# Kernel optimization log

Hardware: AMD Instinct MI355X
Metric: run time of the kernel (lower is better)

Reference implementation:

```python
import jax, jax.numpy as jnp
import numpy as np

D_MODEL = 512
N_HEADS = 8
HEAD_DIM = D_MODEL // N_HEADS
SEQ = 2048
BATCH = 2
EPS = 1e-5
SCALE = 1.0 / np.sqrt(HEAD_DIM).astype(np.float32)
# (kind, window, dilation) per head, matching init_kwargs head_specs
SPECS = [("global", 0, 1), ("global", 0, 1),
         ("window", 64, 1), ("window", 128, 1), ("window", 256, 1),
         ("dilated", 64, 2), ("dilated", 64, 4), ("dilated", 64, 8)]


def build_masks(N):
    i = jnp.arange(N)
    D = jnp.abs(i[:, None] - i[None, :])
    ms = []
    for kind, w, dil in SPECS:
        if kind == "global":
            ms.append(jnp.ones((N, N), dtype=bool))
        elif kind == "window":
            ms.append(D <= w)
        else:  # dilated
            ms.append((D % dil == 0) & (D // dil <= w))
    return jnp.stack(ms)  # [H, N, N] bool


def layernorm(x, g, b):
    mu = jnp.mean(x, axis=-1, keepdims=True)
    var = jnp.mean((x - mu) ** 2, axis=-1, keepdims=True)
    return (x - mu) * jax.lax.rsqrt(var + EPS) * g + b


def setup_inputs() -> dict:
    key = jax.random.key(0)
    ks = jax.random.split(key, 7)
    w = 0.02
    return {
        "x": jax.random.normal(ks[0], (BATCH, SEQ, D_MODEL), dtype=jnp.float32),
        "Wq": jax.random.normal(ks[1], (D_MODEL, D_MODEL), dtype=jnp.float32) * w,
        "Wk": jax.random.normal(ks[2], (D_MODEL, D_MODEL), dtype=jnp.float32) * w,
        "Wv": jax.random.normal(ks[3], (D_MODEL, D_MODEL), dtype=jnp.float32) * w,
        "Wo": jax.random.normal(ks[4], (D_MODEL, D_MODEL), dtype=jnp.float32) * w,
        "T_w1": jax.random.normal(ks[5], (D_MODEL, D_MODEL), dtype=jnp.float32) * w,
        "T_b1": jnp.zeros((D_MODEL,), dtype=jnp.float32),
        "T_w2": jax.random.normal(ks[6], (1, D_MODEL), dtype=jnp.float32) * w,
        "T_b2": jnp.zeros((1,), dtype=jnp.float32),
        "ln_in_g": jnp.ones((D_MODEL,), dtype=jnp.float32),
        "ln_in_b": jnp.zeros((D_MODEL,), dtype=jnp.float32),
        "ln_out_g": jnp.ones((D_MODEL,), dtype=jnp.float32),
        "ln_out_b": jnp.zeros((D_MODEL,), dtype=jnp.float32),
    }


def reference(x, Wq, Wk, Wv, Wo, T_w1, T_b1, T_w2, T_b2,
              ln_in_g, ln_in_b, ln_out_g, ln_out_b):
    B, N, H = x.shape
    x0 = x
    xn = layernorm(x, ln_in_g, ln_in_b)
    # torch Linear: y = x @ W.T ; reshape to [B, h, N, d]
    def heads(W):
        return (xn @ W.T).reshape(B, N, N_HEADS, HEAD_DIM).transpose(0, 2, 1, 3)
    Q, K, V = heads(Wq), heads(Wk), heads(Wv)
    attn = jnp.einsum("bhqd,bhkd->bhqk", Q, K) * SCALE
    mask = build_masks(N)  # [h, N, N]
    attn = jnp.where(mask[None], attn, -jnp.inf)
    attn = jax.nn.softmax(attn, axis=-1)  # every row has diagonal unmasked
    out = jnp.einsum("bhqk,bhkd->bhqd", attn, V)
    out = out.transpose(0, 2, 1, 3).reshape(B, N, N_HEADS * HEAD_DIM)
    out = out @ Wo.T
    # tanh-gated softmax over sequence dim
    T_logits = jnp.tanh(xn @ T_w1.T + T_b1) @ T_w2.T + T_b2  # [B, N, 1]
    T = jax.nn.softmax(T_logits, axis=1)
    out = out * T
    return layernorm(out + x0, ln_out_g, ln_out_b)
```

## Files before the change

kernel.cpp:

```cpp
#include <hip/hip_runtime.h>
#include <math.h>

#define N_SEQ 2048
#define DM    512
#define NTOK  4096
#define NH    8
#define HD    64
#define NSLOT 18

typedef __attribute__((ext_vector_type(8))) short short8;
typedef __attribute__((ext_vector_type(4))) short short4_t;
typedef __attribute__((ext_vector_type(4))) float f32x4;

__device__ inline short f2bf(float x) {
    union { float f; unsigned u; } v; v.f = x;
    unsigned r = v.u + 0x7fff + ((v.u >> 16) & 1);
    return (short)(r >> 16);
}
__device__ inline float bf2f(short s) {
    union { unsigned u; float f; } v; v.u = ((unsigned)(unsigned short)s) << 16;
    return v.f;
}
__device__ inline unsigned pkbf(float a, float b) {
    return ((unsigned)(unsigned short)f2bf(b) << 16) | (unsigned)(unsigned short)f2bf(a);
}
__device__ inline float ftanh(float x) {
    float e = __expf(2.f * x);
    return 1.f - 2.f / (e + 1.f);
}

__device__ inline f32x4 mfma16(short8 a, short8 b, f32x4 c) {
    return __builtin_amdgcn_mfma_f32_16x16x32_bf16(a, b, c, 0, 0, 0);
}

__device__ __forceinline__ void async_cp16(const short* g, short* l) {
    __builtin_amdgcn_global_load_lds(
        (const __attribute__((address_space(1))) void*)g,
        (__attribute__((address_space(3))) void*)l, 16, 0, 0);
}

__global__ __launch_bounds__(256) void k_lncvt(
    const float* __restrict__ x, const float* __restrict__ g,
    const float* __restrict__ b, short* __restrict__ y, float* __restrict__ lg,
    const float* __restrict__ Wq, const float* __restrict__ Wk,
    const float* __restrict__ Wv, const float* __restrict__ Tw1,
    const float* __restrict__ Wo,
    short* __restrict__ wcat, short* __restrict__ wo) {
    int blk = blockIdx.x, t = threadIdx.x;
    if (blk < 2048) {
        int sub = t >> 7, tt = t & 127;
        int tk = blk * 2 + sub;
        if (tt == 0) lg[tk] = 0.f;
        float4 xv = ((const float4*)(x + (size_t)tk * DM))[tt];
        float s = xv.x + xv.y + xv.z + xv.w;
        float q = xv.x*xv.x + xv.y*xv.y + xv.z*xv.z + xv.w*xv.w;
        for (int o = 32; o; o >>= 1) { s += __shfl_down(s, o); q += __shfl_down(q, o); }
        __shared__ float ls[4], lq[4];
        if ((t & 63) == 0) { ls[t >> 6] = s; lq[t >> 6] = q; }
        __syncthreads();
        s = ls[sub * 2] + ls[sub * 2 + 1];
        q = lq[sub * 2] + lq[sub * 2 + 1];
        float mu = s * (1.f / DM);
        float var = q * (1.f / DM) - mu * mu;
        float rs = rsqrtf(var + 1e-5f);
        float4 gv = ((const float4*)g)[tt], bv = ((const float4*)b)[tt];
        short4_t o;
        o[0] = f2bf((xv.x - mu) * rs * gv.x + bv.x);
        o[1] = f2bf((xv.y - mu) * rs * gv.y + bv.y);
        o[2] = f2bf((xv.z - mu) * rs * gv.z + bv.z);
        o[3] = f2bf((xv.w - mu) * rs * gv.w + bv.w);
        *(short4_t*)&y[(size_t)tk * DM + tt * 4] = o;
    } else {
        int id = (blk - 2048) * 256 + t;
        if (id < 262144) {
            int z = id >> 16; int off = id & 65535;
            const float* s = (z == 0) ? Wq : (z == 1) ? Wk : (z == 2) ? Wv : Tw1;
            float4 v = ((const float4*)s)[off];
            short4_t o = {f2bf(v.x), f2bf(v.y), f2bf(v.z), f2bf(v.w)};
            *(short4_t*)(wcat + (size_t)z * 262144 + (size_t)off * 4) = o;
        } else {
            int off = id - 262144;
            float4 v = ((const float4*)Wo)[off];
            short4_t o = {f2bf(v.x), f2bf(v.y), f2bf(v.z), f2bf(v.w)};
            *(short4_t*)(wo + (size_t)off * 4) = o;
        }
    }
}

__global__ __launch_bounds__(256) void k_gemmqkvt(
    const short* __restrict__ A, const short* __restrict__ W,
    const float* __restrict__ Tb1, const float* __restrict__ Tw2,
    short* __restrict__ qb, short* __restrict__ kb, short* __restrict__ vtb,
    float* __restrict__ lg) {
    __shared__ short As[128 * 32];
    __shared__ short Bs[128 * 32];
    int t = threadIdx.x;
    int lane = t & 63, w = t >> 6;
    int wy = w >> 1, wx = w & 1;
    int ln = lane & 15, q4 = lane >> 4;
    int c0 = blockIdx.x * 128, m0 = blockIdx.y * 128;
    int sr = t >> 2, sc = (t & 3) << 3;
    f32x4 acc[4][4];
    f32x4 zero = {0.f, 0.f, 0.f, 0.f};
    #pragma unroll
    for (int i = 0; i < 4; i++)
        #pragma unroll
        for (int j = 0; j < 4; j++) acc[i][j] = zero;
    for (int k0 = 0; k0 < DM; k0 += 32) {
        __syncthreads();
        async_cp16(&A[(size_t)(m0 + sr) * DM + k0 + sc],      &As[sr * 32 + sc]);
        async_cp16(&A[(size_t)(m0 + 64 + sr) * DM + k0 + sc], &As[(64 + sr) * 32 + sc]);
        async_cp16(&W[(size_t)(c0 + sr) * DM + k0 + sc],      &Bs[sr * 32 + sc]);
        async_cp16(&W[(size_t)(c0 + 64 + sr) * DM + k0 + sc], &Bs[(64 + sr) * 32 + sc]);
        __syncthreads();
        short8 af[4], bfr[4];
        #pragma unroll
        for (int i = 0; i < 4; i++)
            af[i] = *(short8*)&As[(wy * 64 + i * 16 + ln) * 32 + q4 * 8];
        #pragma unroll
        for (int j = 0; j < 4; j++)
            bfr[j] = *(short8*)&Bs[(wx * 64 + j * 16 + ln) * 32 + q4 * 8];
        #pragma unroll
        for (int i = 0; i < 4; i++)
            #pragma unroll
            for (int j = 0; j < 4; j++)
                acc[i][j] = mfma16(af[i], bfr[j], acc[i][j]);
    }
    int z = c0 >> 9;
    if (z < 2) {
        short* dst = (z == 0) ? qb : kb;
        float sc2 = (z == 0) ? 0.125f : 1.0f;
        #pragma unroll
        for (int i = 0; i < 4; i++)
            #pragma unroll
            for (int j = 0; j < 4; j++)
                #pragma unroll
                for (int r = 0; r < 4; r++) {
                    int row = m0 + wy * 64 + i * 16 + q4 * 4 + r;
                    int col = c0 + wx * 64 + j * 16 + ln;
                    int nin = col & 511;
                    int h = nin >> 6, d = nin & 63;
                    int bi = row >> 11, n = row & (N_SEQ - 1);
                    dst[(((size_t)bi * NH + h) * N_SEQ + n) * HD + d] =
                        f2bf(acc[i][j][r] * sc2);
                }
    } else if (z == 2) {
        #pragma unroll
        for (int i = 0; i < 4; i++) {
            int row0 = m0 + wy * 64 + i * 16 + q4 * 4;
            int bi = row0 >> 11, n0 = row0 & (N_SEQ - 1);
            #pragma unroll
            for (int j = 0; j < 4; j++) {
                int nin = (c0 + wx * 64 + j * 16 + ln) & 511;
                int h = nin >> 6, d = nin & 63;
                short4_t o = {f2bf(acc[i][j][0]), f2bf(acc[i][j][1]),
                              f2bf(acc[i][j][2]), f2bf(acc[i][j][3])};
                *(short4_t*)&vtb[(((size_t)bi * NH + h) * HD + d) * N_SEQ + n0] = o;
            }
        }
    } else {
        #pragma unroll
        for (int i = 0; i < 4; i++) {
            #pragma unroll
            for (int r = 0; r < 4; r++) {
                float s = 0.f;
                #pragma unroll
                for (int j = 0; j < 4; j++) {
                    int tc = (c0 & 511) + wx * 64 + j * 16 + ln;
                    s += ftanh(acc[i][j][r] + Tb1[tc]) * Tw2[tc];
                }
                s += __shfl_xor(s, 1);
                s += __shfl_xor(s, 2);
                s += __shfl_xor(s, 4);
                s += __shfl_xor(s, 8);
                if (ln == 0) {
                    int row = m0 + wy * 64 + i * 16 + q4 * 4 + r;
                    atomicAdd(&lg[row], s);
                }
            }
        }
    }
}

__global__ __launch_bounds__(256) void k_gemmp(
    const short* __restrict__ A, const short* __restrict__ W,
    float* __restrict__ proj) {
    __shared__ short As[128 * 32];
    __shared__ short Bs[64 * 32];
    int t = threadIdx.x;
    int lane = t & 63, w = t >> 6;
    int wy = w >> 1, wx = w & 1;
    int ln = lane & 15, q4 = lane >> 4;
    int c0 = blockIdx.x * 64, m0 = blockIdx.y * 128;
    int sr = t >> 2, sc = (t & 3) << 3;
    int br = t >> 2, bc = (t & 3) << 3;
    f32x4 acc[4][2];
    f32x4 zero = {0.f, 0.f, 0.f, 0.f};
    #pragma unroll
    for (int i = 0; i < 4; i++) { acc[i][0] = zero; acc[i][1] = zero; }
    for (int k0 = 0; k0 < DM; k0 += 32) {
        __syncthreads();
        async_cp16(&A[(size_t)(m0 + sr) * DM + k0 + sc],      &As[sr * 32 + sc]);
        async_cp16(&A[(size_t)(m0 + 64 + sr) * DM + k0 + sc], &As[(64 + sr) * 32 + sc]);
        if (br < 64)
            async_cp16(&W[(size_t)(c0 + br) * DM + k0 + bc], &Bs[br * 32 + bc]);
        __syncthreads();
        short8 af[4], bfr[2];
        #pragma unroll
        for (int i = 0; i < 4; i++)
            af[i] = *(short8*)&As[(wy * 64 + i * 16 + ln) * 32 + q4 * 8];
        #pragma unroll
        for (int j = 0; j < 2; j++)
            bfr[j] = *(short8*)&Bs[(wx * 32 + j * 16 + ln) * 32 + q4 * 8];
        #pragma unroll
        for (int i = 0; i < 4; i++)
            #pragma unroll
            for (int j = 0; j < 2; j++)
                acc[i][j] = mfma16(af[i], bfr[j], acc[i][j]);
    }
    #pragma unroll
    for (int i = 0; i < 4; i++)
        #pragma unroll
        for (int j = 0; j < 2; j++)
            #pragma unroll
            for (int r = 0; r < 4; r++) {
                int row = m0 + wy * 64 + i * 16 + q4 * 4 + r;
                int col = c0 + wx * 32 + j * 16 + ln;
                proj[(size_t)row * DM + col] = acc[i][j][r];
            }
}

__global__ __launch_bounds__(256) void k_attn(const short* __restrict__ qb,
                                              const short* __restrict__ kb,
                                              const short* __restrict__ vtb,
                                              short* __restrict__ P_O,
                                              float* __restrict__ P_ml) {
    __shared__ short Ks[128 * 72];
    __shared__ short Vt[64 * 136];
    __shared__ short Pa[4][16 * 136];
    int t = threadIdx.x;
    int lane = t & 63, w = t >> 6;
    int ln = lane & 15, q4 = lane >> 4;
    int slot = blockIdx.x, qt = blockIdx.y, bi = blockIdx.z;
    int q0 = qt * 64;
    int h, c;
    if (slot < 4)        { h = 0; c = slot; }
    else if (slot < 8)   { h = 1; c = slot - 4; }
    else if (slot == 8)  { h = 2; c = 0; }
    else if (slot == 9)  { h = 3; c = 0; }
    else if (slot < 12)  { h = 4; c = slot - 10; }
    else if (slot == 12) { h = 5; c = 0; }
    else if (slot < 15)  { h = 6; c = slot - 13; }
    else                 { h = 7; c = slot - 15; }
    int kind = (h < 2) ? 0 : (h < 5) ? 1 : 2;
    int wnd = (h == 2 || h >= 5) ? 64 : (h == 3) ? 128 : (h == 4) ? 256 : 0;
    int dsh = (h == 5) ? 1 : (h == 6) ? 2 : (h == 7) ? 3 : 0;
    int dmask = (1 << dsh) - 1;
    int wmax = (kind == 0) ? 0 : (wnd << dsh);
    int tLoU, tHiU, CS;
    if (kind == 0) { tLoU = 0; tHiU = 15; CS = 4; }
    else { tLoU = (q0 - wmax) >> 7; tHiU = (q0 + 63 + wmax) >> 7; CS = 3; }
    int ktLo = tLoU + c * CS;
    int ktHi = ktLo + CS - 1;
    if (ktHi > tHiU) ktHi = tHiU;
    if (ktHi > 15) ktHi = 15;
    if (ktLo < 0) ktLo = 0;
    int p4 = (bi * 32 + qt) * NSLOT + slot;
    float* ml = P_ml + (size_t)p4 * 128;
    if (ktLo > ktHi) {
        if (t < 64) { ml[t] = -1e30f; ml[64 + t] = 0.f; }
        return;
    }
    const size_t base = ((size_t)bi * NH + h) * N_SEQ * HD;
    const short* Q = qb + base;
    const short* K = kb + base;
    const short* Vg = vtb + base;
    short8 qa[2];
    {
        const short* qrow = Q + (size_t)(q0 + w * 16 + ln) * HD + q4 * 8;
        qa[0] = *(const short8*)qrow;
        qa[1] = *(const short8*)(qrow + 32);
    }
    int qi = q0 + w * 16 + ln;
    float m_i = -1e30f, l_i = 0.f;
    f32x4 OT[4];
    f32x4 zero = {0.f, 0.f, 0.f, 0.f};
    #pragma unroll
    for (int d = 0; d < 4; d++) OT[d] = zero;
    short* Paw = Pa[w];
    int skr = t >> 1, skc = (t & 1) << 3;
    (void)skr; (void)skc;
    short8 kreg[4], vreg[4];
    {
        int k0 = ktLo << 7;
        #pragma unroll
        for (int i2 = 0; i2 < 4; i2++) {
            int id = t + 256 * i2;
            int kr = id >> 3, cc = id & 7;
            kreg[i2] = *(const short8*)&K[(size_t)(k0 + kr) * HD + cc * 8];
            int dr = id >> 4, kc = id & 15;
            vreg[i2] = *(const short8*)&Vg[(size_t)dr * N_SEQ + k0 + kc * 8];
        }
    }
    for (int kt = ktLo; kt <= ktHi; kt++) {
        int k0 = kt << 7;
        __syncthreads();
        #pragma unroll
        for (int i2 = 0; i2 < 4; i2++) {
            int id = t + 256 * i2;
            int kr = id >> 3, cc = id & 7;
            *(short8*)&Ks[kr * 72 + cc * 8] = kreg[i2];
            int dr = id >> 4, kc = id & 15;
            *(short8*)&Vt[dr * 136 + kc * 8] = vreg[i2];
        }
        __syncthreads();
        if (kt < ktHi) {
            int kn = (kt + 1) << 7;
            #pragma unroll
            for (int i2 = 0; i2 < 4; i2++) {
                int id = t + 256 * i2;
                int kr = id >> 3, cc = id & 7;
                kreg[i2] = *(const short8*)&K[(size_t)(kn + kr) * HD + cc * 8];
                int dr = id >> 4, kc = id & 15;
                vreg[i2] = *(const short8*)&Vg[(size_t)dr * N_SEQ + kn + kc * 8];
            }
        }
        f32x4 ST[8];
        #pragma unroll
        for (int nt = 0; nt < 8; nt++) ST[nt] = zero;
        #pragma unroll
        for (int nt = 0; nt < 8; nt++) {
            #pragma unroll
            for (int ks = 0; ks < 2; ks++) {
                short8 af = *(short8*)&Ks[(nt * 16 + ln) * 72 + ks * 32 + q4 * 8];
                ST[nt] = mfma16(af, qa[ks], ST[nt]);
            }
        }
        if (kind != 0) {
            #pragma unroll
            for (int nt = 0; nt < 8; nt++)
                #pragma unroll
                for (int r = 0; r < 4; r++) {
                    int key = k0 + nt * 16 + q4 * 4 + r;
                    int dlt = qi - key; dlt = (dlt < 0) ? -dlt : dlt;
                    int valid;
                    if (kind == 1) valid = (dlt <= wnd);
                    else valid = ((dlt & dmask) == 0) && ((dlt >> dsh) <= wnd);
                    if (!valid) ST[nt][r] = -1e30f;
                }
        }
        float rm = -1e30f;
        #pragma unroll
        for (int nt = 0; nt < 8; nt++) {
            float a = fmaxf(ST[nt][0], ST[nt][1]);
            float b = fmaxf(ST[nt][2], ST[nt][3]);
            rm = fmaxf(rm, fmaxf(a, b));
        }
        rm = fmaxf(rm, __shfl_xor(rm, 16));
        rm = fmaxf(rm, __shfl_xor(rm, 32));
        float mn = fmaxf(m_i, rm);
        float sc = __expf(m_i - mn);
        float rs = 0.f;
        #pragma unroll
        for (int nt = 0; nt < 8; nt++) {
            float p0 = __expf(ST[nt][0] - mn);
            float p1 = __expf(ST[nt][1] - mn);
            float p2 = __expf(ST[nt][2] - mn);
            float p3 = __expf(ST[nt][3] - mn);
            rs += (p0 + p1) + (p2 + p3);
            *(unsigned*)&Paw[ln * 136 + nt * 16 + q4 * 4]     = pkbf(p0, p1);
            *(unsigned*)&Paw[ln * 136 + nt * 16 + q4 * 4 + 2] = pkbf(p2, p3);
        }
        rs += __shfl_xor(rs, 16);
        rs += __shfl_xor(rs, 32);
        l_i = l_i * sc + rs;
        m_i = mn;
        #pragma unroll
        for (int d = 0; d < 4; d++) OT[d] *= sc;
        short8 pb[4];
        #pragma unroll
        for (int ks = 0; ks < 4; ks++)
            pb[ks] = *(short8*)&Paw[ln * 136 + ks * 32 + q4 * 8];
        #pragma unroll
        for (int dt = 0; dt < 4; dt++) {
            #pragma unroll
            for (int ks = 0; ks < 4; ks++) {
                short8 a = *(short8*)&Vt[(dt * 16 + ln) * 136 + ks * 32 + q4 * 8];
                OT[dt] = mfma16(a, pb[ks], OT[dt]);
            }
        }
    }
    if (q4 == 0) { ml[w * 16 + ln] = m_i; ml[64 + w * 16 + ln] = l_i; }
    #pragma unroll
    for (int dt = 0; dt < 4; dt++) {
        *(unsigned*)&Paw[ln * 136 + dt * 16 + q4 * 4]     = pkbf(OT[dt][0], OT[dt][1]);
        *(unsigned*)&Paw[ln * 136 + dt * 16 + q4 * 4 + 2] = pkbf(OT[dt][2], OT[dt][3]);
    }
    short8 o0 = *(short8*)&Paw[ln * 136 + q4 * 16];
    short8 o1 = *(short8*)&Paw[ln * 136 + q4 * 16 + 8];
    short* Op = P_O + (size_t)p4 * 4096;
    *(short8*)&Op[(w * 16 + ln) * 64 + q4 * 16] = o0;
    *(short8*)&Op[(w * 16 + ln) * 64 + q4 * 16 + 8] = o1;
}

__global__ __launch_bounds__(256) void k_combgate(const short* __restrict__ P_O,
                                                  const float* __restrict__ P_ml,
                                                  short* __restrict__ ob,
                                                  const float* __restrict__ lg,
                                                  float* __restrict__ gate) {
    int blk = blockIdx.x, t = threadIdx.x;
    if (blk < 512) {
        const int hbase[8] = {0, 4, 8, 9, 10, 12, 13, 15};
        const int hcnt[8]  = {4, 4, 1, 1, 2, 1, 2, 3};
        int h = blk & 7, qt = (blk >> 3) & 31, bi = blk >> 8;
        int row = t >> 2, c0 = (t & 3) * 16;
        int pb = (bi * 32 + qt) * NSLOT + hbase[h];
        int cnt = hcnt[h];
        float m = -1e30f;
        for (int s = 0; s < cnt; s++)
            m = fmaxf(m, P_ml[(size_t)(pb + s) * 128 + row]);
        float l = 0.f;
        float acc[16];
        #pragma unroll
        for (int j = 0; j < 16; j++) acc[j] = 0.f;
        for (int s = 0; s < cnt; s++) {
            float ms = P_ml[(size_t)(pb + s) * 128 + row];
            float ls = P_ml[(size_t)(pb + s) * 128 + 64 + row];
            if (ls > 0.f) {
                float sc = __expf(ms - m);
                l += ls * sc;
                const short* Op = P_O + (size_t)(pb + s) * 4096 + row * 64 + c0;
                short8 v0 = *(const short8*)Op;
                short8 v1 = *(const short8*)(Op + 8);
                #pragma unroll
                for (int j = 0; j < 8; j++) acc[j]     += bf2f(v0[j]) * sc;
                #pragma unroll
                for (int j = 0; j < 8; j++) acc[8 + j] += bf2f(v1[j]) * sc;
            }
        }
        float inv = 1.f / l;
        int n = qt * 64 + row;
        short8 o0, o1;
        #pragma unroll
        for (int j = 0; j < 8; j++) o0[j] = f2bf(acc[j] * inv);
        #pragma unroll
        for (int j = 0; j < 8; j++) o1[j] = f2bf(acc[8 + j] * inv);
        short* dst = ob + ((size_t)bi * N_SEQ + n) * DM + h * 64 + c0;
        *(short8*)dst = o0;
        *(short8*)(dst + 8) = o1;
    } else {
        __shared__ float rg[8];
        int b = blk - 512;
        float v[8];
        {
            float4 a0 = *(const float4*)&lg[b * N_SEQ + t * 8];
            float4 a1 = *(const float4*)&lg[b * N_SEQ + t * 8 + 4];
            v[0] = a0.x; v[1] = a0.y; v[2] = a0.z; v[3] = a0.w;
            v[4] = a1.x; v[5] = a1.y; v[6] = a1.z; v[7] = a1.w;
        }
        float m = v[0];
        #pragma unroll
        for (int j = 1; j < 8; j++) m = fmaxf(m, v[j]);
        for (int o = 32; o; o >>= 1) m = fmaxf(m, __shfl_down(m, o));
        if ((t & 63) == 0) rg[t >> 6] = m;
        __syncthreads();
        m = fmaxf(fmaxf(rg[0], rg[1]), fmaxf(rg[2], rg[3]));
        float e[8], s = 0.f;
        #pragma unroll
        for (int j = 0; j < 8; j++) { e[j] = __expf(v[j] - m); s += e[j]; }
        for (int o = 32; o; o >>= 1) s += __shfl_down(s, o);
        if ((t & 63) == 0) rg[4 + (t >> 6)] = s;
        __syncthreads();
        s = (rg[4] + rg[5]) + (rg[6] + rg[7]);
        float inv = 1.f / s;
        float4 o0 = {e[0] * inv, e[1] * inv, e[2] * inv, e[3] * inv};
        float4 o1 = {e[4] * inv, e[5] * inv, e[6] * inv, e[7] * inv};
        *(float4*)&gate[b * N_SEQ + t * 8] = o0;
        *(float4*)&gate[b * N_SEQ + t * 8 + 4] = o1;
    }
}

__global__ __launch_bounds__(128) void k_final(const float* __restrict__ proj,
                                               const float* __restrict__ gate,
                                               const float* __restrict__ x0,
                                               const float* __restrict__ g,
                                               const float* __restrict__ b,
                                               float* __restrict__ out) {
    int tk = blockIdx.x, t = threadIdx.x;
    float gt = gate[tk];
    float4 pv = ((const float4*)(proj + (size_t)tk * DM))[t];
    float4 xv = ((const float4*)(x0 + (size_t)tk * DM))[t];
    float4 y;
    y.x = pv.x * gt + xv.x;
    y.y = pv.y * gt + xv.y;
    y.z = pv.z * gt + xv.z;
    y.w = pv.w * gt + xv.w;
    float s = y.x + y.y + y.z + y.w;
    float q = y.x*y.x + y.y*y.y + y.z*y.z + y.w*y.w;
    for (int o = 32; o; o >>= 1) { s += __shfl_down(s, o); q += __shfl_down(q, o); }
    __shared__ float ls[2], lq[2];
    if ((t & 63) == 0) { ls[t >> 6] = s; lq[t >> 6] = q; }
    __syncthreads();
    s = ls[0] + ls[1]; q = lq[0] + lq[1];
    float mu = s * (1.f / DM);
    float var = q * (1.f / DM) - mu * mu;
    float rs = rsqrtf(var + 1e-5f);
    float4 gv = ((const float4*)g)[t], bv = ((const float4*)b)[t];
    float4 o;
    o.x = (y.x - mu) * rs * gv.x + bv.x;
    o.y = (y.y - mu) * rs * gv.y + bv.y;
    o.z = (y.z - mu) * rs * gv.z + bv.z;
    o.w = (y.w - mu) * rs * gv.w + bv.w;
    ((float4*)(out + (size_t)tk * DM))[t] = o;
}

extern "C" void kernel_launch(void* const* d_in, const int* in_sizes, int n_in,
                              void* d_out, int out_size, void* d_ws, size_t ws_size,
                              hipStream_t stream) {
    (void)in_sizes; (void)n_in; (void)out_size; (void)ws_size;
    const float* x    = (const float*)d_in[0];
    const float* Wq   = (const float*)d_in[1];
    const float* Wk   = (const float*)d_in[2];
    const float* Wv   = (const float*)d_in[3];
    const float* Wo   = (const float*)d_in[4];
    const float* Tw1  = (const float*)d_in[5];
    const float* Tb1  = (const float*)d_in[6];
    const float* Tw2  = (const float*)d_in[7];
    const float* ling = (const float*)d_in[9];
    const float* linb = (const float*)d_in[10];
    const float* logg = (const float*)d_in[11];
    const float* logb = (const float*)d_in[12];
    float* out = (float*)d_out;

    const size_t SZ = (size_t)NTOK * DM;
    const int NPART = 2 * 32 * NSLOT;
    char* p = (char*)d_ws;
    short* xn   = (short*)p; p += SZ * 2;
    short* wcat = (short*)p; p += (size_t)2048 * DM * 2;
    short* wo   = (short*)p; p += (size_t)DM * DM * 2;
    short* qb   = (short*)p; p += SZ * 2;
    short* kb   = (short*)p; p += SZ * 2;
    short* vtb  = (short*)p; p += SZ * 2;
    short* obuf = (short*)p; p += SZ * 2;
    float* lg   = (float*)p; p += (size_t)NTOK * 4;
    float* gate = (float*)p; p += (size_t)NTOK * 4;
    float* P_ml = (float*)p; p += (size_t)NPART * 128 * 4;
    float* proj = (float*)p;
    short* P_O  = (short*)p; p += (size_t)NPART * 4096 * 2;

    k_lncvt<<<3328, 256, 0, stream>>>(x, ling, linb, xn, lg,
                                      Wq, Wk, Wv, Tw1, Wo, wcat, wo);
    k_gemmqkvt<<<dim3(16, 32), 256, 0, stream>>>(xn, wcat, Tb1, Tw2,
                                                 qb, kb, vtb, lg);
    k_attn<<<dim3(NSLOT, 32, 2), 256, 0, stream>>>(qb, kb, vtb, P_O, P_ml);
    k_combgate<<<514, 256, 0, stream>>>(P_O, P_ml, obuf, lg, gate);
    k_gemmp<<<dim3(8, 32), 256, 0, stream>>>(obuf, wo, proj);
    k_final<<<NTOK, 128, 0, stream>>>(proj, gate, x, logg, logb, out);
}
```

Baseline: 162.9 us.

## Fuse output projection with gating, residual and final layernorm; stage V-transpose via LDS

Replaces the separate output-projection GEMM and final layernorm kernels with one kernel. Each 32-row block computes all 512 output columns, applies the gate and residual, and reduces layernorm statistics through shared memory. This removes the fp32 proj round trip and one launch. The trade-offs are only 128 blocks, each reloading the full Wo tile per k-step, which lowers parallelism. Separately, the V-transpose store in the QKV GEMM now goes through an LDS buffer so the global writes are wide and coalesced.

```diff
diff --git a/kernel.cpp b/kernel.cpp
--- a/kernel.cpp
+++ b/kernel.cpp
@@ -92,8 +92,12 @@
     const float* __restrict__ Tb1, const float* __restrict__ Tw2,
     short* __restrict__ qb, short* __restrict__ kb, short* __restrict__ vtb,
     float* __restrict__ lg) {
-    __shared__ short As[128 * 32];
-    __shared__ short Bs[128 * 32];
+    __shared__ union {
+        struct { short As[128 * 32]; short Bs[128 * 32]; } s;
+        short Ct[128 * 132];
+    } u;
+    short* As = u.s.As;
+    short* Bs = u.s.Bs;
     int t = threadIdx.x;
     int lane = t & 63, w = t >> 6;
     int wy = w >> 1, wx = w & 1;
@@ -145,18 +149,27 @@
                         f2bf(acc[i][j][r] * sc2);
                 }
     } else if (z == 2) {
-        #pragma unroll
-        for (int i = 0; i < 4; i++) {
-            int row0 = m0 + wy * 64 + i * 16 + q4 * 4;
-            int bi = row0 >> 11, n0 = row0 & (N_SEQ - 1);
+        __syncthreads();
+        #pragma unroll
+        for (int i = 0; i < 4; i++)
             #pragma unroll
             for (int j = 0; j < 4; j++) {
-                int nin = (c0 + wx * 64 + j * 16 + ln) & 511;
-                int h = nin >> 6, d = nin & 63;
+                int lcol = wx * 64 + j * 16 + ln;
+                int lrow = wy * 64 + i * 16 + q4 * 4;
                 short4_t o = {f2bf(acc[i][j][0]), f2bf(acc[i][j][1]),
                               f2bf(acc[i][j][2]), f2bf(acc[i][j][3])};
-                *(short4_t*)&vtb[(((size_t)bi * NH + h) * HD + d) * N_SEQ + n0] = o;
-            }
+                *(short4_t*)&u.Ct[lcol * 132 + lrow] = o;
+            }
+        __syncthreads();
+        int bi = m0 >> 11, n0 = m0 & (N_SEQ - 1);
+        #pragma unroll
+        for (int it = 0; it < 8; it++) {
+            int id = t + 256 * it;
+            int lcol = id >> 4, ch = id & 15;
+            int nin = (c0 & 511) + lcol;
+            int h = nin >> 6, d = nin & 63;
+            short8 v = *(short8*)&u.Ct[lcol * 132 + ch * 8];
+            *(short8*)&vtb[(((size_t)bi * NH + h) * HD + d) * N_SEQ + n0 + ch * 8] = v;
         }
     } else {
         #pragma unroll
@@ -180,54 +193,6 @@
             }
         }
     }
-}
-
-__global__ __launch_bounds__(256) void k_gemmp(
-    const short* __restrict__ A, const short* __restrict__ W,
-    float* __restrict__ proj) {
-    __shared__ short As[128 * 32];
-    __shared__ short Bs[64 * 32];
-    int t = threadIdx.x;
-    int lane = t & 63, w = t >> 6;
-    int wy = w >> 1, wx = w & 1;
-    int ln = lane & 15, q4 = lane >> 4;
-    int c0 = blockIdx.x * 64, m0 = blockIdx.y * 128;
-    int sr = t >> 2, sc = (t & 3) << 3;
-    int br = t >> 2, bc = (t & 3) << 3;
-    f32x4 acc[4][2];
-    f32x4 zero = {0.f, 0.f, 0.f, 0.f};
-    #pragma unroll
-    for (int i = 0; i < 4; i++) { acc[i][0] = zero; acc[i][1] = zero; }
-    for (int k0 = 0; k0 < DM; k0 += 32) {
-        __syncthreads();
-        async_cp16(&A[(size_t)(m0 + sr) * DM + k0 + sc],      &As[sr * 32 + sc]);
-        async_cp16(&A[(size_t)(m0 + 64 + sr) * DM + k0 + sc], &As[(64 + sr) * 32 + sc]);
-        if (br < 64)
-            async_cp16(&W[(size_t)(c0 + br) * DM + k0 + bc], &Bs[br * 32 + bc]);
-        __syncthreads();
-        short8 af[4], bfr[2];
-        #pragma unroll
-        for (int i = 0; i < 4; i++)
-            af[i] = *(short8*)&As[(wy * 64 + i * 16 + ln) * 32 + q4 * 8];
-        #pragma unroll
-        for (int j = 0; j < 2; j++)
-            bfr[j] = *(short8*)&Bs[(wx * 32 + j * 16 + ln) * 32 + q4 * 8];
-        #pragma unroll
-        for (int i = 0; i < 4; i++)
-            #pragma unroll
-            for (int j = 0; j < 2; j++)
-                acc[i][j] = mfma16(af[i], bfr[j], acc[i][j]);
-    }
-    #pragma unroll
-    for (int i = 0; i < 4; i++)
-        #pragma unroll
-        for (int j = 0; j < 2; j++)
-            #pragma unroll
-            for (int r = 0; r < 4; r++) {
-                int row = m0 + wy * 64 + i * 16 + q4 * 4 + r;
-                int col = c0 + wx * 32 + j * 16 + ln;
-                proj[(size_t)row * DM + col] = acc[i][j][r];
-            }
 }
 
 __global__ __launch_bounds__(256) void k_attn(const short* __restrict__ qb,
@@ -288,8 +253,6 @@
     #pragma unroll
     for (int d = 0; d < 4; d++) OT[d] = zero;
     short* Paw = Pa[w];
-    int skr = t >> 1, skc = (t & 1) << 3;
-    (void)skr; (void)skc;
     short8 kreg[4], vreg[4];
     {
         int k0 = ktLo << 7;
@@ -480,38 +443,110 @@
     }
 }
 
-__global__ __launch_bounds__(128) void k_final(const float* __restrict__ proj,
-                                               const float* __restrict__ gate,
-                                               const float* __restrict__ x0,
-                                               const float* __restrict__ g,
-                                               const float* __restrict__ b,
-                                               float* __restrict__ out) {
-    int tk = blockIdx.x, t = threadIdx.x;
-    float gt = gate[tk];
-    float4 pv = ((const float4*)(proj + (size_t)tk * DM))[t];
-    float4 xv = ((const float4*)(x0 + (size_t)tk * DM))[t];
-    float4 y;
-    y.x = pv.x * gt + xv.x;
-    y.y = pv.y * gt + xv.y;
-    y.z = pv.z * gt + xv.z;
-    y.w = pv.w * gt + xv.w;
-    float s = y.x + y.y + y.z + y.w;
-    float q = y.x*y.x + y.y*y.y + y.z*y.z + y.w*y.w;
-    for (int o = 32; o; o >>= 1) { s += __shfl_down(s, o); q += __shfl_down(q, o); }
-    __shared__ float ls[2], lq[2];
-    if ((t & 63) == 0) { ls[t >> 6] = s; lq[t >> 6] = q; }
+__global__ __launch_bounds__(256) void k_gemmpf(
+    const short* __restrict__ A,
+    const short* __restrict__ W,
+    const float* __restrict__ gate,
+    const float* __restrict__ x0,
+    const float* __restrict__ g,
+    const float* __restrict__ b,
+    float* __restrict__ out) {
+    __shared__ short As[32 * 32];
+    __shared__ short Bs[512 * 32];
+    __shared__ float redS[32][4], redQ[32][4];
+    int t = threadIdx.x;
+    int lane = t & 63, w = t >> 6;
+    int ln = lane & 15, q4 = lane >> 4;
+    int m0 = blockIdx.x * 32;
+    f32x4 acc[2][8];
+    f32x4 zero = {0.f, 0.f, 0.f, 0.f};
+    #pragma unroll
+    for (int i = 0; i < 2; i++)
+        #pragma unroll
+        for (int j = 0; j < 8; j++) acc[i][j] = zero;
+    for (int k0 = 0; k0 < DM; k0 += 32) {
+        __syncthreads();
+        if (t < 128) {
+            int r = t >> 2, c = (t & 3) << 3;
+            async_cp16(&A[(size_t)(m0 + r) * DM + k0 + c], &As[r * 32 + c]);
+        }
+        #pragma unroll
+        for (int it = 0; it < 8; it++) {
+            int id = t + 256 * it;
+            int r = id >> 2, c = (id & 3) << 3;
+            async_cp16(&W[(size_t)r * DM + k0 + c], &Bs[r * 32 + c]);
+        }
+        __syncthreads();
+        short8 af[2];
+        af[0] = *(short8*)&As[(ln) * 32 + q4 * 8];
+        af[1] = *(short8*)&As[(16 + ln) * 32 + q4 * 8];
+        #pragma unroll
+        for (int j = 0; j < 8; j++) {
+            short8 bfr = *(short8*)&Bs[(w * 128 + j * 16 + ln) * 32 + q4 * 8];
+            acc[0][j] = mfma16(af[0], bfr, acc[0][j]);
+            acc[1][j] = mfma16(af[1], bfr, acc[1][j]);
+        }
+    }
+    float gts[2][4];
+    #pragma unroll
+    for (int i = 0; i < 2; i++)
+        #pragma unroll
+        for (int r = 0; r < 4; r++)
+            gts[i][r] = gate[m0 + i * 16 + q4 * 4 + r];
+    float sS[2][4] = {}, sQ[2][4] = {};
+    #pragma unroll
+    for (int i = 0; i < 2; i++)
+        #pragma unroll
+        for (int j = 0; j < 8; j++) {
+            int col = w * 128 + j * 16 + ln;
+            #pragma unroll
+            for (int r = 0; r < 4; r++) {
+                int row = m0 + i * 16 + q4 * 4 + r;
+                float y = acc[i][j][r] * gts[i][r] + x0[(size_t)row * DM + col];
+                acc[i][j][r] = y;
+                sS[i][r] += y;
+                sQ[i][r] += y * y;
+            }
+        }
+    #pragma unroll
+    for (int o = 1; o < 16; o <<= 1) {
+        #pragma unroll
+        for (int i = 0; i < 2; i++)
+            #pragma unroll
+            for (int r = 0; r < 4; r++) {
+                sS[i][r] += __shfl_xor(sS[i][r], o);
+                sQ[i][r] += __shfl_xor(sQ[i][r], o);
+            }
+    }
+    if (ln == 0) {
+        #pragma unroll
+        for (int i = 0; i < 2; i++)
+            #pragma unroll
+            for (int r = 0; r < 4; r++) {
+                redS[i * 16 + q4 * 4 + r][w] = sS[i][r];
+                redQ[i * 16 + q4 * 4 + r][w] = sQ[i][r];
+            }
+    }
     __syncthreads();
-    s = ls[0] + ls[1]; q = lq[0] + lq[1];
-    float mu = s * (1.f / DM);
-    float var = q * (1.f / DM) - mu * mu;
-    float rs = rsqrtf(var + 1e-5f);
-    float4 gv = ((const float4*)g)[t], bv = ((const float4*)b)[t];
-    float4 o;
-    o.x = (y.x - mu) * rs * gv.x + bv.x;
-    o.y = (y.y - mu) * rs * gv.y + bv.y;
-    o.z = (y.z - mu) * rs * gv.z + bv.z;
-    o.w = (y.w - mu) * rs * gv.w + bv.w;
-    ((float4*)(out + (size_t)tk * DM))[t] = o;
+    #pragma unroll
+    for (int i = 0; i < 2; i++) {
+        #pragma unroll
+        for (int r = 0; r < 4; r++) {
+            int lr = i * 16 + q4 * 4 + r;
+            float S = (redS[lr][0] + redS[lr][1]) + (redS[lr][2] + redS[lr][3]);
+            float Qq = (redQ[lr][0] + redQ[lr][1]) + (redQ[lr][2] + redQ[lr][3]);
+            float mu = S * (1.f / DM);
+            float var = Qq * (1.f / DM) - mu * mu;
+            float rsq = rsqrtf(var + 1e-5f);
+            int row = m0 + lr;
+            #pragma unroll
+            for (int j = 0; j < 8; j++) {
+                int col = w * 128 + j * 16 + ln;
+                out[(size_t)row * DM + col] =
+                    (acc[i][j][r] - mu) * rsq * g[col] + b[col];
+            }
+        }
+    }
 }
 
 extern "C" void kernel_launch(void* const* d_in, const int* in_sizes, int n_in,
@@ -545,7 +580,6 @@
     float* lg   = (float*)p; p += (size_t)NTOK * 4;
     float* gate = (float*)p; p += (size_t)NTOK * 4;
     float* P_ml = (float*)p; p += (size_t)NPART * 128 * 4;
-    float* proj = (float*)p;
     short* P_O  = (short*)p; p += (size_t)NPART * 4096 * 2;
 
     k_lncvt<<<3328, 256, 0, stream>>>(x, ling, linb, xn, lg,
@@ -554,6 +588,5 @@
                                                  qb, kb, vtb, lg);
     k_attn<<<dim3(NSLOT, 32, 2), 256, 0, stream>>>(qb, kb, vtb, P_O, P_ml);
     k_combgate<<<514, 256, 0, stream>>>(P_O, P_ml, obuf, lg, gate);
-    k_gemmp<<<dim3(8, 32), 256, 0, stream>>>(obuf, wo, proj);
-    k_final<<<NTOK, 128, 0, stream>>>(proj, gate, x, logg, logb, out);
-}
+    k_gemmpf<<<128, 256, 0, stream>>>(obuf, wo, gate, x, logg, logb, out);
+}
```

Result: no change. 165.5 us (+1.6%).
